# Optimization experiments

Measured on AMD Instinct MI355X. Metric: run time of the kernel, lower is better.

## Reference

```python
import jax, jax.numpy as jnp
import numpy as np
from jax import lax

TIME_DIM = 100   # time_feat_dim
MEM_DIM = 172    # node_feat_dim == memory_dim
TAU = 0.3        # energy_threshold
LAM = 0.01       # softshrink sparsity_threshold


def _layer_norm(x, w, b, eps=1e-5):
    m = x.mean(-1, keepdims=True)
    v = ((x - m) ** 2).mean(-1, keepdims=True)
    return (x - m) / jnp.sqrt(v + eps) * w + b


def _time_encode(t):
    # TGN time encoder: cos(t * 1/10^linspace(0,9,D)), fixed (non-trainable)
    freqs = 1.0 / (10.0 ** jnp.linspace(0.0, 9.0, TIME_DIM))
    return jnp.cos(t[..., None] * freqs)


def _softshrink(x, lam=LAM):
    return jnp.where(x > lam, x - lam, jnp.where(x < -lam, x + lam, 0.0))


def setup_inputs() -> dict:
    key = jax.random.key(0)
    ks = jax.random.split(key, 12)
    B, N, NUM_NODES = 8192, 32, 500000
    s = 0.02  # scale used by Global_Local_Filtering
    return {
        "node_ids": jnp.arange(B, dtype=jnp.int32),
        "neighbor_node_ids": jax.random.randint(ks[0], (B, N), 0, NUM_NODES, dtype=jnp.int32),
        "node_interact_times": jax.random.uniform(ks[1], (B,), dtype=jnp.float32) * 1000.0,
        "neighbor_times": jax.random.uniform(ks[2], (B, N), dtype=jnp.float32) * 1000.0,
        "node_memories": jnp.zeros((NUM_NODES, MEM_DIM), jnp.float32),
        "r1": s * jax.random.normal(ks[3], (TIME_DIM, MEM_DIM), jnp.float32),
        "i1": s * jax.random.normal(ks[4], (TIME_DIM, MEM_DIM), jnp.float32),
        "rb1": s * jax.random.normal(ks[5], (MEM_DIM,), jnp.float32),
        "ib1": s * jax.random.normal(ks[6], (MEM_DIM,), jnp.float32),
        "conv_w": 0.02 * jax.random.normal(ks[7], (MEM_DIM, MEM_DIM, 8), jnp.float32),
        "conv_b": 0.02 * jax.random.normal(ks[8], (MEM_DIM,), jnp.float32),
        "rhythm_w": 0.1 * jax.random.normal(ks[9], (272, 1, 4), jnp.float32),
        "lin_w": 0.05 * jax.random.normal(ks[10], (272, MEM_DIM), jnp.float32),
        "lin_b": 0.02 * jax.random.normal(ks[11], (MEM_DIM,), jnp.float32),
        "mb_ln_w": jnp.ones((MEM_DIM,), jnp.float32),
        "mb_ln_b": jnp.zeros((MEM_DIM,), jnp.float32),
        "ln_w": jnp.ones((MEM_DIM,), jnp.float32),
        "ln_b": jnp.zeros((MEM_DIM,), jnp.float32),
    }


def reference(node_ids, neighbor_node_ids, node_interact_times, neighbor_times,
              node_memories, r1, i1, rb1, ib1, conv_w, conv_b,
              rhythm_w, lin_w, lin_b, mb_ln_w, mb_ln_b, ln_w, ln_b):
    # ---- RhythmMemoryUpdater.update_memory ----
    messages = _time_encode(node_interact_times)                 # [B,100]
    old_mem = node_memories[node_ids]                            # [B,172] gather
    x = jnp.concatenate([messages, old_mem], axis=-1)[:, :, None]  # [B,272,1] (NCH)
    # depthwise Conv1d(272,272,k=4,pad=2,groups=272,no bias): length 1 -> 2
    x = lax.conv_general_dilated(x, rhythm_w, (1,), [(2, 2)],
                                 dimension_numbers=("NCH", "OIH", "NCH"),
                                 feature_group_count=272)        # [B,272,2]
    x = jnp.einsum("bcl,cd->bld", x, lin_w) + lin_b              # [B,2,172]
    new_mem = x.mean(axis=1)                                     # mean(dim=1) since 2 != memory_dim
    # set_memories: layer_norm then scatter; then gather + SeqFilter layernorm
    updated = node_memories.at[node_ids].set(_layer_norm(new_mem, mb_ln_w, mb_ln_b))
    gathered = lax.stop_gradient(updated[node_ids])              # memory bank is non-trainable (no_grad)
    root_node_time = _layer_norm(gathered, ln_w, ln_b)           # [B,172]

    # ---- neighbor branch: FSTS (Global_Local_Filtering + Conv1d) ----
    dt = node_interact_times[:, None] - neighbor_times           # [B,N]
    tfeat = _time_encode(dt)                                     # [B,N,100]
    tfeat = jnp.where((neighbor_node_ids == 0)[..., None], 0.0, tfeat)

    xf = jnp.fft.fft(tfeat, axis=1, norm="ortho")                # [B,N,100] complex
    energy = jnp.sum(jnp.abs(xf) ** 2, axis=-1)                  # [B,N]
    mask = (energy / (energy.mean() + 1e-6) >= TAU).astype(tfeat.dtype)
    low = xf * mask[..., None]
    o_r = jnp.einsum("bnc,cd->bnd", low.real, r1) - jnp.einsum("bnc,cd->bnd", low.imag, i1) + rb1
    o_i = jnp.einsum("bnc,cd->bnd", low.imag, r1) + jnp.einsum("bnc,cd->bnd", low.real, i1) + ib1
    y_fft = _softshrink(jax.nn.relu(o_r)) + 1j * _softshrink(jax.nn.relu(o_i))
    y = jnp.fft.ifft(y_fft, axis=1, norm="ortho").real           # [B,N,172]

    # Local_Correlation: Conv1d(172,172,k=8,pad=4) over neighbor axis, then mean over length
    yc = lax.conv_general_dilated(y.transpose(0, 2, 1), conv_w, (1,), [(4, 4)],
                                  dimension_numbers=("NCH", "OIH", "NCH"))
    yc = yc + conv_b[None, :, None]                              # [B,172,33]
    neighbor_out = yc.mean(axis=-1)                              # [B,172]

    return root_node_time + neighbor_out
```

## Files before the change

### kernel.cpp

```cpp
#include <hip/hip_runtime.h>
#include <hip/hip_bf16.h>
#include <math.h>

#define B_ 8192
#define NN 32
#define TD 100
#define MD 172
#define KD 1376
#define TAUC 0.3f
#define LAMC 0.01f

typedef __attribute__((ext_vector_type(8))) short short8;
typedef __attribute__((ext_vector_type(4))) float f32x4;

#define WS_U_OFF    256
#define U_BYTES     ((size_t)B_ * KD * 2)
#define CONVB_ELEMS (11 * 43 * 64 * 8)
#define WBIG_ELEMS  (22 * 7 * 64 * 8)
#define CS_ELEMS    (2 * 64 * 8)
#define ROOT_ELEMS  (11 * 9 * 64 * 8)
#define CS2_ELEMS   (4 * 64 * 8)
#define FRAG_SHORTS (CONVB_ELEMS + WBIG_ELEMS + CS_ELEMS + ROOT_ELEMS + CS2_ELEMS)
#define TBL_ELEMS   164

__device__ __forceinline__ float wred(float v) {
#pragma unroll
  for (int o = 32; o > 0; o >>= 1) v += __shfl_down(v, o, 64);
  return v;
}

__device__ __forceinline__ short bf16_bits(float f) {
  __hip_bfloat16 h = __float2bfloat16(f);
  return *(short*)&h;
}

__device__ __forceinline__ unsigned pack2(float a, float b) {
  return (unsigned)(unsigned short)bf16_bits(a) |
         ((unsigned)(unsigned short)bf16_bits(b) << 16);
}

__device__ __forceinline__ float fcos(float x) {
  float r = x * 0.15915494309189535f;
  r = r - floorf(r);
  return __builtin_amdgcn_cosf(r);
}

__global__ __launch_bounds__(256) void k_prep0(
    const float* __restrict__ conv_w, const float* __restrict__ r1,
    const float* __restrict__ i1, const float* __restrict__ rhythm_w,
    const float* __restrict__ lin_w, short* __restrict__ convB,
    short* __restrict__ Wfrag, short* __restrict__ CSfrag,
    short* __restrict__ Rfrag, short* __restrict__ CS2frag,
    float* __restrict__ tbl) {
  int idx = blockIdx.x * 256 + threadIdx.x;
  const float inv_s = 0.17677669529663687f;
  if (idx < CONVB_ELEMS) {
    int j = idx & 7;
    int l = (idx >> 3) & 63;
    int s = (idx >> 9) % 43;
    int n0 = idx / (43 * 64 * 8);
    int k = s * 32 + (l >> 4) * 8 + j;
    int col = n0 * 16 + (l & 15);
    float v = (col < MD) ? conv_w[(long)col * KD + k] : 0.f;
    convB[idx] = bf16_bits(v);
    return;
  }
  idx -= CONVB_ELEMS;
  if (idx < WBIG_ELEMS) {
    int j = idx & 7;
    int l = (idx >> 3) & 63;
    int s = (idx % 3584) >> 9;
    int n0 = idx / 3584;
    int k = s * 32 + (l >> 4) * 8 + j;
    int col = n0 * 16 + (l & 15);
    float v = 0.f;
    if (k < 200) {
      if (n0 < 11) {
        int d = col;
        if (d < MD) v = (k < 100) ? r1[k * MD + d] : -i1[(k - 100) * MD + d];
      } else {
        int d = col - 176;
        if (d >= 0 && d < MD) v = (k < 100) ? i1[k * MD + d] : r1[(k - 100) * MD + d];
      }
    }
    Wfrag[idx] = bf16_bits(v);
    return;
  }
  idx -= WBIG_ELEMS;
  if (idx < CS_ELEMS) {
    int j = idx & 7;
    int l = (idx >> 3) & 63;
    int s = idx >> 9;
    int row = l & 15;
    int kq = s * 32 + (l >> 4) * 8 + j;
    float v = 0.f;
    if (row < 8) {
      int kp = (kq < 32) ? kq : kq - 32;
      int lo = row - 4; if (lo < 0) lo = 0;
      int hi = row + 28; if (hi > 31) hi = 31;
      double cs = 0.0, ss = 0.0;
      for (int n = lo; n <= hi; ++n) {
        double ang = 0.19634954084936207740 * (double)((kp * n) & 31);
        cs += cos(ang); ss += sin(ang);
      }
      v = ((kq < 32) ? (float)cs : -(float)ss) * inv_s;
    }
    CSfrag[idx] = bf16_bits(v);
    return;
  }
  idx -= CS_ELEMS;
  if (idx < ROOT_ELEMS) {
    int n = idx / 4608;
    int rem = idx % 4608;
    int s = rem >> 9;
    int l = (rem >> 3) & 63;
    int j = rem & 7;
    int k = s * 32 + (l >> 4) * 8 + j;
    int col = n * 16 + (l & 15);
    float v = 0.f;
    if (k < 272 && col < MD) {
      float hw = 0.5f * (rhythm_w[k * 4 + 1] + rhythm_w[k * 4 + 2]);
      v = hw * lin_w[k * MD + col];
    }
    Rfrag[idx] = bf16_bits(v);
    return;
  }
  idx -= ROOT_ELEMS;
  if (idx < CS2_ELEMS) {
    int set = idx >> 9, l = (idx >> 3) & 63, j = idx & 7;
    int mt = set >> 1, isS = set & 1;
    int kf = mt * 16 + (l & 15);
    int n = ((l >> 4) << 3) + j;
    double ang = 0.19634954084936207740 * (double)((kf * n) & 31);
    double v = isS ? -sin(ang) : cos(ang);
    CS2frag[idx] = bf16_bits((float)(v * 0.1767766952966368811));
    return;
  }
  idx -= CS2_ELEMS;
  if (idx < TBL_ELEMS) {
    float v;
    if (idx < 100)      v = (float)exp(-9.0 * (double)idx / 99.0 * 2.302585092994045684);
    else if (idx < 132) v = (float)cos(0.19634954084936207740 * (double)(idx - 100));
    else                v = (float)sin(0.19634954084936207740 * (double)(idx - 132));
    tbl[idx] = v;
  }
}

__global__ __launch_bounds__(256) void k_mean(const int* __restrict__ nid,
                                              const float* __restrict__ t,
                                              const float* __restrict__ nt,
                                              const float* __restrict__ tbl,
                                              float* __restrict__ ws) {
  __shared__ float fr[TD];
  __shared__ float part[4];
  int tid = threadIdx.x;
  if (tid < TD) fr[tid] = tbl[tid];
  __syncthreads();
  int idx = blockIdx.x * 256 + tid;
  int b = idx >> 5;
  float s = 0.f;
  if (nid[idx] != 0) {
    float dt = t[b] - nt[idx];
    for (int c = 0; c < TD; ++c) { float v = fcos(dt * fr[c]); s = fmaf(v, v, s); }
  }
  s = wred(s);
  if ((tid & 63) == 0) part[tid >> 6] = s;
  __syncthreads();
  if (tid == 0) atomicAdd(ws, part[0] + part[1] + part[2] + part[3]);
}

__global__ __launch_bounds__(384, 8) void k_main(
    const int* __restrict__ nbr_id, const float* __restrict__ t,
    const float* __restrict__ nt, const float* __restrict__ rb1,
    const float* __restrict__ ib1, const float* __restrict__ ws0,
    const short* __restrict__ Wfrag, const short* __restrict__ CSfrag,
    const short* __restrict__ CS2frag, const float* __restrict__ tbl,
    short* __restrict__ u_out) {
  __shared__ __align__(16) short sA[32 * 232];
  __shared__ __align__(16) unsigned char s_un[12800];
  __shared__ float s_fr[TD];
  __shared__ float s_dt[32], s_z[32];
  __shared__ float s_energy[32];

  short* sB = (short*)s_un;
  short* Y = (short*)s_un;
  const int tid = threadIdx.x;
  const int b = blockIdx.x;
  const int l = tid & 63, w = tid >> 6;
  const int c = l & 15, q = l >> 4;

  if (tid < 32) {
    int gi = b * NN + tid;
    int id = nbr_id[gi];
    float d = t[b] - nt[gi];
    s_z[tid]  = (id == 0) ? 0.f : 1.f;
    s_dt[tid] = (id == 0) ? 0.f : d;
    s_energy[tid] = 0.f;
  }
  if (tid < TD) s_fr[tid] = tbl[tid];
  __syncthreads();

  for (int idx = tid; idx < 3584; idx += 384) {
    int tt = idx >> 9, ll = (idx >> 3) & 63, j = idx & 7;
    int n = ((ll >> 4) << 3) + j;
    int cc = (tt << 4) + (ll & 15);
    float v = (cc < TD) ? s_z[n] * fcos(s_dt[n] * s_fr[cc]) : 0.f;
    sB[idx] = bf16_bits(v);
  }
  if (tid < 256) {
    int row = tid >> 3, qq = tid & 7;
    *(uint2*)(sA + row * 232 + 200 + qq * 4) = make_uint2(0u, 0u);
  }
  __syncthreads();

  const int mside = (w >= 3) ? 1 : 0;
  const int wn = w % 3;
  {
    short8 Ac = *(const short8*)(CS2frag + (((mside << 1) + 0) << 9) + (l << 3));
    short8 As = *(const short8*)(CS2frag + (((mside << 1) + 1) << 9) + (l << 3));
    float e4[4] = {0.f, 0.f, 0.f, 0.f};
    for (int tt = wn; tt < 7; tt += 3) {
      short8 Bt = *(const short8*)(sB + (tt << 9) + (l << 3));
      f32x4 xr = (f32x4)(0.f), xi = (f32x4)(0.f);
      xr = __builtin_amdgcn_mfma_f32_16x16x32_bf16(Ac, Bt, xr, 0, 0, 0);
      xi = __builtin_amdgcn_mfma_f32_16x16x32_bf16(As, Bt, xi, 0, 0, 0);
      int cc = (tt << 4) + c;
      if (cc < TD) {
#pragma unroll
        for (int r = 0; r < 4; ++r) {
          int k = mside * 16 + q * 4 + r;
          sA[k * 232 + cc]       = bf16_bits(xr[r]);
          sA[k * 232 + 100 + cc] = bf16_bits(xi[r]);
          e4[r] = fmaf(xr[r], xr[r], e4[r]);
          e4[r] = fmaf(xi[r], xi[r], e4[r]);
        }
      }
    }
#pragma unroll
    for (int m = 1; m < 16; m <<= 1) {
#pragma unroll
      for (int r = 0; r < 4; ++r) e4[r] += __shfl_xor(e4[r], m, 64);
    }
    if (c == 0) {
#pragma unroll
      for (int r = 0; r < 4; ++r)
        atomicAdd(&s_energy[mside * 16 + q * 4 + r], e4[r]);
    }
  }
  __syncthreads();

  {
    float gth = TAUC * (ws0[0] * (1.0f / 262144.0f) + 1e-6f);
    for (int idx = tid; idx < 800; idx += 384) {
      int row = idx / 25, qq = idx - row * 25;
      if (s_energy[row] < gth)
        *(uint4*)((char*)sA + row * 464 + qq * 16) = make_uint4(0u,0u,0u,0u);
    }
  }
  __syncthreads();

#pragma unroll
  for (int rep = 0; rep < 2; ++rep) {
    int n = w + 6 * rep;
    if (n < 11) {
      f32x4 acc0 = (f32x4)(0.f), acc1 = (f32x4)(0.f);
#pragma unroll
      for (int s = 0; s < 7; ++s) {
        short8 bb = *(const short8*)(Wfrag + (((n * 7 + s) << 6) + l) * 8);
        short8 a0 = *(const short8*)(sA + c * 232 + (q << 3) + s * 32);
        short8 a1 = *(const short8*)(sA + (16 + c) * 232 + (q << 3) + s * 32);
        acc0 = __builtin_amdgcn_mfma_f32_16x16x32_bf16(a0, bb, acc0, 0, 0, 0);
        acc1 = __builtin_amdgcn_mfma_f32_16x16x32_bf16(a1, bb, acc1, 0, 0, 0);
      }
      int d = n * 16 + c;
      bool valid = (d < MD);
      float bias = valid ? rb1[d] : 0.f;
      f32x4 y0, y1;
#pragma unroll
      for (int r = 0; r < 4; ++r) {
        y0[r] = valid ? fmaxf(acc0[r] + bias - LAMC, 0.f) : 0.f;
        y1[r] = valid ? fmaxf(acc1[r] + bias - LAMC, 0.f) : 0.f;
      }
      *(uint2*)(Y + d * 32 + (q << 2))      = make_uint2(pack2(y0[0], y0[1]), pack2(y0[2], y0[3]));
      *(uint2*)(Y + d * 32 + 16 + (q << 2)) = make_uint2(pack2(y1[0], y1[1]), pack2(y1[2], y1[3]));
    }
  }
  __syncthreads();

  f32x4 uacc[2];
  uacc[0] = (f32x4)(0.f); uacc[1] = (f32x4)(0.f);
  {
    short8 cs0 = *(const short8*)(CSfrag + (l << 3));
#pragma unroll
    for (int ti = 0; ti < 2; ++ti) {
      int nu = w + 6 * ti;
      if (nu < 11) {
        short8 bfr = *(const short8*)(Y + (nu * 16 + c) * 32 + (q << 3));
        uacc[ti] = __builtin_amdgcn_mfma_f32_16x16x32_bf16(cs0, bfr, uacc[ti], 0, 0, 0);
      }
    }
  }
  __syncthreads();

#pragma unroll
  for (int rep = 0; rep < 2; ++rep) {
    int n = w + 6 * rep;
    if (n < 11) {
      int nw = n + 11;
      f32x4 acc0 = (f32x4)(0.f), acc1 = (f32x4)(0.f);
#pragma unroll
      for (int s = 0; s < 7; ++s) {
        short8 bb = *(const short8*)(Wfrag + (((nw * 7 + s) << 6) + l) * 8);
        short8 a0 = *(const short8*)(sA + c * 232 + (q << 3) + s * 32);
        short8 a1 = *(const short8*)(sA + (16 + c) * 232 + (q << 3) + s * 32);
        acc0 = __builtin_amdgcn_mfma_f32_16x16x32_bf16(a0, bb, acc0, 0, 0, 0);
        acc1 = __builtin_amdgcn_mfma_f32_16x16x32_bf16(a1, bb, acc1, 0, 0, 0);
      }
      int d = n * 16 + c;
      bool valid = (d < MD);
      float bias = valid ? ib1[d] : 0.f;
      f32x4 y0, y1;
#pragma unroll
      for (int r = 0; r < 4; ++r) {
        y0[r] = valid ? fmaxf(acc0[r] + bias - LAMC, 0.f) : 0.f;
        y1[r] = valid ? fmaxf(acc1[r] + bias - LAMC, 0.f) : 0.f;
      }
      *(uint2*)(Y + d * 32 + (q << 2))      = make_uint2(pack2(y0[0], y0[1]), pack2(y0[2], y0[3]));
      *(uint2*)(Y + d * 32 + 16 + (q << 2)) = make_uint2(pack2(y1[0], y1[1]), pack2(y1[2], y1[3]));
    }
  }
  __syncthreads();

  {
    short8 cs1 = *(const short8*)(CSfrag + ((64 + l) << 3));
#pragma unroll
    for (int ti = 0; ti < 2; ++ti) {
      int nu = w + 6 * ti;
      if (nu < 11) {
        short8 bfr = *(const short8*)(Y + (nu * 16 + c) * 32 + (q << 3));
        uacc[ti] = __builtin_amdgcn_mfma_f32_16x16x32_bf16(cs1, bfr, uacc[ti], 0, 0, 0);
        int d = nu * 16 + c;
        if (q < 2 && d < MD) {
          uint2 pv = make_uint2(pack2(uacc[ti][0], uacc[ti][1]),
                                pack2(uacc[ti][2], uacc[ti][3]));
          *(uint2*)(u_out + (long)b * KD + d * 8 + q * 4) = pv;
        }
      }
    }
  }
}

__global__ __launch_bounds__(1024) void k_tail(
    const int* __restrict__ node_ids, const float* __restrict__ t,
    const float* __restrict__ node_mem, const short* __restrict__ u,
    const short* __restrict__ convB, const float* __restrict__ conv_b,
    const short* __restrict__ Rfrag, const float* __restrict__ lin_b,
    const float* __restrict__ mb_w, const float* __restrict__ mb_b,
    const float* __restrict__ ln_w, const float* __restrict__ ln_b,
    const float* __restrict__ tbl, float* __restrict__ out) {
  __shared__ __align__(16) short aR[16 * 296];
  __shared__ __align__(16) float Ct[16 * 176];
  const int tid = threadIdx.x;
  const int l = tid & 63, w = tid >> 6;
  const int c = l & 15, q = l >> 4;
  const int b0 = blockIdx.x * 16;

  for (int idx = tid; idx < 16 * 296; idx += 1024) {
    int r = idx / 296, cc = idx - r * 296;
    float v = 0.f;
    if (cc < TD) v = fcos(t[b0 + r] * tbl[cc]);
    else if (cc < 272) v = node_mem[(long)node_ids[b0 + r] * MD + (cc - TD)];
    aR[idx] = bf16_bits(v);
  }
  __syncthreads();

  f32x4 cacc = (f32x4)(0.f);
  if (w < 11) {
    const short* ap = u + (long)(b0 + c) * KD + (q << 3);
    const short* bp = convB + (((long)w * 43) * 64 + l) * 8;
#pragma unroll 4
    for (int s = 0; s < 43; ++s) {
      short8 a = *(const short8*)(ap + s * 32);
      short8 bb = *(const short8*)(bp + (s << 9));
      cacc = __builtin_amdgcn_mfma_f32_16x16x32_bf16(a, bb, cacc, 0, 0, 0);
    }
  } else {
    const int rstart = (w - 11) * 2;
    const int rcnt = (w == 15) ? 3 : 2;
    f32x4 racc[3];
#pragma unroll
    for (int tt = 0; tt < 3; ++tt) racc[tt] = (f32x4)(0.f);
    const short* arp = aR + c * 296 + (q << 3);
    for (int s = 0; s < 9; ++s) {
      short8 a = *(const short8*)(arp + s * 32);
#pragma unroll
      for (int tt = 0; tt < 3; ++tt) {
        if (tt < rcnt) {
          int n = rstart + tt;
          short8 bb = *(const short8*)(Rfrag + (((n * 9 + s) * 64) + l) * 8);
          racc[tt] = __builtin_amdgcn_mfma_f32_16x16x32_bf16(a, bb, racc[tt], 0, 0, 0);
        }
      }
    }
#pragma unroll
    for (int tt = 0; tt < 3; ++tt) {
      if (tt < rcnt) {
        int n = (rstart + tt) * 16 + c;
#pragma unroll
        for (int r = 0; r < 4; ++r)
          Ct[(q * 4 + r) * 176 + n] = racc[tt][r];
      }
    }
  }
  __syncthreads();

  if (tid < 256) {
    int r = tid >> 4, g = tid & 15;
    float v[11];
    float sm = 0.f, sq = 0.f;
#pragma unroll
    for (int j = 0; j < 11; ++j) {
      int cc = g + 16 * j;
      float x = (cc < MD) ? (Ct[r * 176 + cc] + lin_b[cc]) : 0.f;
      v[j] = x; sm += x; sq += x * x;
    }
#pragma unroll
    for (int m = 1; m < 16; m <<= 1) { sm += __shfl_xor(sm, m, 64); sq += __shfl_xor(sq, m, 64); }
    float mean = sm / 172.f;
    float rstd = rsqrtf(sq / 172.f - mean * mean + 1e-5f);
    float sm2 = 0.f, sq2 = 0.f;
#pragma unroll
    for (int j = 0; j < 11; ++j) {
      int cc = g + 16 * j;
      if (cc < MD) {
        float h = (v[j] - mean) * rstd * mb_w[cc] + mb_b[cc];
        v[j] = h; sm2 += h; sq2 += h * h;
      }
    }
#pragma unroll
    for (int m = 1; m < 16; m <<= 1) { sm2 += __shfl_xor(sm2, m, 64); sq2 += __shfl_xor(sq2, m, 64); }
    float mean2 = sm2 / 172.f;
    float rstd2 = rsqrtf(sq2 / 172.f - mean2 * mean2 + 1e-5f);
#pragma unroll
    for (int j = 0; j < 11; ++j) {
      int cc = g + 16 * j;
      if (cc < MD) Ct[r * 176 + cc] = (v[j] - mean2) * rstd2 * ln_w[cc] + ln_b[cc];
    }
  }
  __syncthreads();

  if (w < 11) {
    int n = w * 16 + c;
    if (n < MD) {
      float cb = conv_b[n];
#pragma unroll
      for (int r = 0; r < 4; ++r) {
        int mr = q * 4 + r;
        out[(long)(b0 + mr) * MD + n] =
            Ct[mr * 176 + n] + cacc[r] * (1.0f / 33.0f) + cb;
      }
    }
  }
}

extern "C" void kernel_launch(void* const* d_in, const int* in_sizes, int n_in,
                              void* d_out, int out_size, void* d_ws, size_t ws_size,
                              hipStream_t stream) {
  const int* node_ids = (const int*)d_in[0];
  const int* nbr_id   = (const int*)d_in[1];
  const float* t  = (const float*)d_in[2];
  const float* nt = (const float*)d_in[3];
  const float* node_mem = (const float*)d_in[4];
  const float* r1 = (const float*)d_in[5];
  const float* i1 = (const float*)d_in[6];
  const float* rb1 = (const float*)d_in[7];
  const float* ib1 = (const float*)d_in[8];
  const float* conv_w = (const float*)d_in[9];
  const float* conv_b = (const float*)d_in[10];
  const float* rhythm_w = (const float*)d_in[11];
  const float* lin_w = (const float*)d_in[12];
  const float* lin_b = (const float*)d_in[13];
  const float* mb_w = (const float*)d_in[14];
  const float* mb_b = (const float*)d_in[15];
  const float* ln_w = (const float*)d_in[16];
  const float* ln_b = (const float*)d_in[17];
  float* out = (float*)d_out;
  float* wsf = (float*)d_ws;

  char* base = (char*)d_ws;
  short* u       = (short*)(base + WS_U_OFF);
  short* convB   = (short*)(base + WS_U_OFF + U_BYTES);
  short* Wfrag   = convB + CONVB_ELEMS;
  short* CSfrag  = Wfrag + WBIG_ELEMS;
  short* Rfrag   = CSfrag + CS_ELEMS;
  short* CS2frag = Rfrag + ROOT_ELEMS;
  float* tbl     = (float*)(CS2frag + CS2_ELEMS);

  hipMemsetAsync(d_ws, 0, 16, stream);
  k_prep0<<<(FRAG_SHORTS + TBL_ELEMS + 255) / 256, 256, 0, stream>>>(
      conv_w, r1, i1, rhythm_w, lin_w, convB, Wfrag, CSfrag, Rfrag, CS2frag, tbl);
  k_mean<<<1024, 256, 0, stream>>>(nbr_id, t, nt, tbl, wsf);
  k_main<<<B_, 384, 0, stream>>>(nbr_id, t, nt, rb1, ib1, wsf,
                                 Wfrag, CSfrag, CS2frag, tbl, u);
  k_tail<<<512, 1024, 0, stream>>>(node_ids, t, node_mem, u, convB, conv_b,
                                   Rfrag, lin_b, mb_w, mb_b, ln_w, ln_b, tbl, out);
}
```

Baseline: 565.1 us.

## Fuse real/imag spectral GEMMs with fp32 cos/sin reduction and merge prep kernels

The prep and energy-mean kernels are merged into one launch, with the mean blocks computing their frequency table inline. In the main kernel, the real and imaginary output GEMMs now run in a single pass with four accumulators. The inverse-DFT-plus-conv-window projection is done in registers: an fp32 dot product against a shared-memory cos/sin table, then cross-lane shuffles. This removes the bf16 Y staging buffer, two block barriers and two small MFMA stages, in exchange for more registers per thread and extra shuffles.

```diff
diff --git a/kernel.cpp b/kernel.cpp
--- a/kernel.cpp
+++ b/kernel.cpp
@@ -17,11 +17,12 @@
 #define U_BYTES     ((size_t)B_ * KD * 2)
 #define CONVB_ELEMS (11 * 43 * 64 * 8)
 #define WBIG_ELEMS  (22 * 7 * 64 * 8)
-#define CS_ELEMS    (2 * 64 * 8)
 #define ROOT_ELEMS  (11 * 9 * 64 * 8)
 #define CS2_ELEMS   (4 * 64 * 8)
-#define FRAG_SHORTS (CONVB_ELEMS + WBIG_ELEMS + CS_ELEMS + ROOT_ELEMS + CS2_ELEMS)
-#define TBL_ELEMS   164
+#define TBL_ELEMS   676
+#define PREP_ITEMS  (CONVB_ELEMS + WBIG_ELEMS + ROOT_ELEMS + CS2_ELEMS + TBL_ELEMS)
+#define MEAN_BLOCKS 1024
+#define PREP_BLOCKS ((PREP_ITEMS + 255) / 256)
 
 __device__ __forceinline__ float wred(float v) {
 #pragma unroll
@@ -45,15 +46,36 @@
   return __builtin_amdgcn_cosf(r);
 }
 
-__global__ __launch_bounds__(256) void k_prep0(
+__global__ __launch_bounds__(256) void k_pm(
+    const int* __restrict__ nid, const float* __restrict__ t,
+    const float* __restrict__ nt,
     const float* __restrict__ conv_w, const float* __restrict__ r1,
     const float* __restrict__ i1, const float* __restrict__ rhythm_w,
     const float* __restrict__ lin_w, short* __restrict__ convB,
-    short* __restrict__ Wfrag, short* __restrict__ CSfrag,
-    short* __restrict__ Rfrag, short* __restrict__ CS2frag,
-    float* __restrict__ tbl) {
-  int idx = blockIdx.x * 256 + threadIdx.x;
+    short* __restrict__ Wfrag, short* __restrict__ Rfrag,
+    short* __restrict__ CS2frag, float* __restrict__ tbl,
+    float* __restrict__ ws) {
   const float inv_s = 0.17677669529663687f;
+  const int tid = threadIdx.x;
+  if (blockIdx.x < MEAN_BLOCKS) {
+    __shared__ float fr[TD];
+    __shared__ float part[4];
+    if (tid < TD) fr[tid] = (float)exp(-9.0 * (double)tid / 99.0 * 2.302585092994045684);
+    __syncthreads();
+    int idx = blockIdx.x * 256 + tid;
+    int b = idx >> 5;
+    float s = 0.f;
+    if (nid[idx] != 0) {
+      float dt = t[b] - nt[idx];
+      for (int c = 0; c < TD; ++c) { float v = fcos(dt * fr[c]); s = fmaf(v, v, s); }
+    }
+    s = wred(s);
+    if ((tid & 63) == 0) part[tid >> 6] = s;
+    __syncthreads();
+    if (tid == 0) atomicAdd(ws, part[0] + part[1] + part[2] + part[3]);
+    return;
+  }
+  int idx = (blockIdx.x - MEAN_BLOCKS) * 256 + tid;
   if (idx < CONVB_ELEMS) {
     int j = idx & 7;
     int l = (idx >> 3) & 63;
@@ -87,28 +109,6 @@
     return;
   }
   idx -= WBIG_ELEMS;
-  if (idx < CS_ELEMS) {
-    int j = idx & 7;
-    int l = (idx >> 3) & 63;
-    int s = idx >> 9;
-    int row = l & 15;
-    int kq = s * 32 + (l >> 4) * 8 + j;
-    float v = 0.f;
-    if (row < 8) {
-      int kp = (kq < 32) ? kq : kq - 32;
-      int lo = row - 4; if (lo < 0) lo = 0;
-      int hi = row + 28; if (hi > 31) hi = 31;
-      double cs = 0.0, ss = 0.0;
-      for (int n = lo; n <= hi; ++n) {
-        double ang = 0.19634954084936207740 * (double)((kp * n) & 31);
-        cs += cos(ang); ss += sin(ang);
-      }
-      v = ((kq < 32) ? (float)cs : -(float)ss) * inv_s;
-    }
-    CSfrag[idx] = bf16_bits(v);
-    return;
-  }
-  idx -= CS_ELEMS;
   if (idx < ROOT_ELEMS) {
     int n = idx / 4608;
     int rem = idx % 4608;
@@ -141,49 +141,37 @@
     float v;
     if (idx < 100)      v = (float)exp(-9.0 * (double)idx / 99.0 * 2.302585092994045684);
     else if (idx < 132) v = (float)cos(0.19634954084936207740 * (double)(idx - 100));
-    else                v = (float)sin(0.19634954084936207740 * (double)(idx - 132));
+    else if (idx < 164) v = (float)sin(0.19634954084936207740 * (double)(idx - 132));
+    else {
+      int i2 = idx - 164;
+      int half = (i2 >= 256) ? 1 : 0;
+      int r = i2 & 255;
+      int k2 = r >> 5, kp = r & 31;
+      int lo = k2 - 4; if (lo < 0) lo = 0;
+      int hi = k2 + 28; if (hi > 31) hi = 31;
+      double cs = 0.0, ss = 0.0;
+      for (int n = lo; n <= hi; ++n) {
+        double ang = 0.19634954084936207740 * (double)((kp * n) & 31);
+        cs += cos(ang); ss += sin(ang);
+      }
+      v = (half ? (float)ss : (float)cs) * inv_s;
+    }
     tbl[idx] = v;
   }
-}
-
-__global__ __launch_bounds__(256) void k_mean(const int* __restrict__ nid,
-                                              const float* __restrict__ t,
-                                              const float* __restrict__ nt,
-                                              const float* __restrict__ tbl,
-                                              float* __restrict__ ws) {
-  __shared__ float fr[TD];
-  __shared__ float part[4];
-  int tid = threadIdx.x;
-  if (tid < TD) fr[tid] = tbl[tid];
-  __syncthreads();
-  int idx = blockIdx.x * 256 + tid;
-  int b = idx >> 5;
-  float s = 0.f;
-  if (nid[idx] != 0) {
-    float dt = t[b] - nt[idx];
-    for (int c = 0; c < TD; ++c) { float v = fcos(dt * fr[c]); s = fmaf(v, v, s); }
-  }
-  s = wred(s);
-  if ((tid & 63) == 0) part[tid >> 6] = s;
-  __syncthreads();
-  if (tid == 0) atomicAdd(ws, part[0] + part[1] + part[2] + part[3]);
 }
 
 __global__ __launch_bounds__(384, 8) void k_main(
     const int* __restrict__ nbr_id, const float* __restrict__ t,
     const float* __restrict__ nt, const float* __restrict__ rb1,
     const float* __restrict__ ib1, const float* __restrict__ ws0,
-    const short* __restrict__ Wfrag, const short* __restrict__ CSfrag,
-    const short* __restrict__ CS2frag, const float* __restrict__ tbl,
-    short* __restrict__ u_out) {
+    const short* __restrict__ Wfrag, const short* __restrict__ CS2frag,
+    const float* __restrict__ tbl, short* __restrict__ u_out) {
   __shared__ __align__(16) short sA[32 * 232];
-  __shared__ __align__(16) unsigned char s_un[12800];
+  __shared__ __align__(16) short sB[3584];
+  __shared__ __align__(16) float s_cs[512];
   __shared__ float s_fr[TD];
-  __shared__ float s_dt[32], s_z[32];
-  __shared__ float s_energy[32];
-
-  short* sB = (short*)s_un;
-  short* Y = (short*)s_un;
+  __shared__ float s_dt[32], s_z[32], s_energy[32];
+
   const int tid = threadIdx.x;
   const int b = blockIdx.x;
   const int l = tid & 63, w = tid >> 6;
@@ -198,6 +186,7 @@
     s_energy[tid] = 0.f;
   }
   if (tid < TD) s_fr[tid] = tbl[tid];
+  for (int i = tid; i < 512; i += 384) s_cs[i] = tbl[164 + i];
   __syncthreads();
 
   for (int idx = tid; idx < 3584; idx += 384) {
@@ -263,88 +252,56 @@
   for (int rep = 0; rep < 2; ++rep) {
     int n = w + 6 * rep;
     if (n < 11) {
-      f32x4 acc0 = (f32x4)(0.f), acc1 = (f32x4)(0.f);
+      f32x4 aR0 = (f32x4)(0.f), aR1 = (f32x4)(0.f);
+      f32x4 aI0 = (f32x4)(0.f), aI1 = (f32x4)(0.f);
 #pragma unroll
       for (int s = 0; s < 7; ++s) {
-        short8 bb = *(const short8*)(Wfrag + (((n * 7 + s) << 6) + l) * 8);
+        short8 br = *(const short8*)(Wfrag + (((n * 7 + s) << 6) + l) * 8);
+        short8 bi = *(const short8*)(Wfrag + ((((n + 11) * 7 + s) << 6) + l) * 8);
         short8 a0 = *(const short8*)(sA + c * 232 + (q << 3) + s * 32);
         short8 a1 = *(const short8*)(sA + (16 + c) * 232 + (q << 3) + s * 32);
-        acc0 = __builtin_amdgcn_mfma_f32_16x16x32_bf16(a0, bb, acc0, 0, 0, 0);
-        acc1 = __builtin_amdgcn_mfma_f32_16x16x32_bf16(a1, bb, acc1, 0, 0, 0);
+        aR0 = __builtin_amdgcn_mfma_f32_16x16x32_bf16(a0, br, aR0, 0, 0, 0);
+        aR1 = __builtin_amdgcn_mfma_f32_16x16x32_bf16(a1, br, aR1, 0, 0, 0);
+        aI0 = __builtin_amdgcn_mfma_f32_16x16x32_bf16(a0, bi, aI0, 0, 0, 0);
+        aI1 = __builtin_amdgcn_mfma_f32_16x16x32_bf16(a1, bi, aI1, 0, 0, 0);
       }
       int d = n * 16 + c;
       bool valid = (d < MD);
-      float bias = valid ? rb1[d] : 0.f;
-      f32x4 y0, y1;
+      float br_ = valid ? rb1[d] : 0.f;
+      float bi_ = valid ? ib1[d] : 0.f;
 #pragma unroll
       for (int r = 0; r < 4; ++r) {
-        y0[r] = valid ? fmaxf(acc0[r] + bias - LAMC, 0.f) : 0.f;
-        y1[r] = valid ? fmaxf(acc1[r] + bias - LAMC, 0.f) : 0.f;
-      }
-      *(uint2*)(Y + d * 32 + (q << 2))      = make_uint2(pack2(y0[0], y0[1]), pack2(y0[2], y0[3]));
-      *(uint2*)(Y + d * 32 + 16 + (q << 2)) = make_uint2(pack2(y1[0], y1[1]), pack2(y1[2], y1[3]));
-    }
-  }
-  __syncthreads();
-
-  f32x4 uacc[2];
-  uacc[0] = (f32x4)(0.f); uacc[1] = (f32x4)(0.f);
-  {
-    short8 cs0 = *(const short8*)(CSfrag + (l << 3));
-#pragma unroll
-    for (int ti = 0; ti < 2; ++ti) {
-      int nu = w + 6 * ti;
-      if (nu < 11) {
-        short8 bfr = *(const short8*)(Y + (nu * 16 + c) * 32 + (q << 3));
-        uacc[ti] = __builtin_amdgcn_mfma_f32_16x16x32_bf16(cs0, bfr, uacc[ti], 0, 0, 0);
-      }
-    }
-  }
-  __syncthreads();
-
-#pragma unroll
-  for (int rep = 0; rep < 2; ++rep) {
-    int n = w + 6 * rep;
-    if (n < 11) {
-      int nw = n + 11;
-      f32x4 acc0 = (f32x4)(0.f), acc1 = (f32x4)(0.f);
-#pragma unroll
-      for (int s = 0; s < 7; ++s) {
-        short8 bb = *(const short8*)(Wfrag + (((nw * 7 + s) << 6) + l) * 8);
-        short8 a0 = *(const short8*)(sA + c * 232 + (q << 3) + s * 32);
-        short8 a1 = *(const short8*)(sA + (16 + c) * 232 + (q << 3) + s * 32);
-        acc0 = __builtin_amdgcn_mfma_f32_16x16x32_bf16(a0, bb, acc0, 0, 0, 0);
-        acc1 = __builtin_amdgcn_mfma_f32_16x16x32_bf16(a1, bb, acc1, 0, 0, 0);
-      }
-      int d = n * 16 + c;
-      bool valid = (d < MD);
-      float bias = valid ? ib1[d] : 0.f;
-      f32x4 y0, y1;
-#pragma unroll
-      for (int r = 0; r < 4; ++r) {
-        y0[r] = valid ? fmaxf(acc0[r] + bias - LAMC, 0.f) : 0.f;
-        y1[r] = valid ? fmaxf(acc1[r] + bias - LAMC, 0.f) : 0.f;
-      }
-      *(uint2*)(Y + d * 32 + (q << 2))      = make_uint2(pack2(y0[0], y0[1]), pack2(y0[2], y0[3]));
-      *(uint2*)(Y + d * 32 + 16 + (q << 2)) = make_uint2(pack2(y1[0], y1[1]), pack2(y1[2], y1[3]));
-    }
-  }
-  __syncthreads();
-
-  {
-    short8 cs1 = *(const short8*)(CSfrag + ((64 + l) << 3));
-#pragma unroll
-    for (int ti = 0; ti < 2; ++ti) {
-      int nu = w + 6 * ti;
-      if (nu < 11) {
-        short8 bfr = *(const short8*)(Y + (nu * 16 + c) * 32 + (q << 3));
-        uacc[ti] = __builtin_amdgcn_mfma_f32_16x16x32_bf16(cs1, bfr, uacc[ti], 0, 0, 0);
-        int d = nu * 16 + c;
-        if (q < 2 && d < MD) {
-          uint2 pv = make_uint2(pack2(uacc[ti][0], uacc[ti][1]),
-                                pack2(uacc[ti][2], uacc[ti][3]));
-          *(uint2*)(u_out + (long)b * KD + d * 8 + q * 4) = pv;
+        aR0[r] = fmaxf(aR0[r] + br_ - LAMC, 0.f);
+        aR1[r] = fmaxf(aR1[r] + br_ - LAMC, 0.f);
+        aI0[r] = fmaxf(aI0[r] + bi_ - LAMC, 0.f);
+        aI1[r] = fmaxf(aI1[r] + bi_ - LAMC, 0.f);
+      }
+      float uk[8];
+#pragma unroll
+      for (int k2 = 0; k2 < 8; ++k2) {
+        f32x4 ct0 = *(const f32x4*)(s_cs + k2 * 32 + (q << 2));
+        f32x4 ct1 = *(const f32x4*)(s_cs + k2 * 32 + 16 + (q << 2));
+        f32x4 st0 = *(const f32x4*)(s_cs + 256 + k2 * 32 + (q << 2));
+        f32x4 st1 = *(const f32x4*)(s_cs + 256 + k2 * 32 + 16 + (q << 2));
+        float sacc = 0.f;
+#pragma unroll
+        for (int r = 0; r < 4; ++r) {
+          sacc = fmaf(ct0[r],  aR0[r], sacc);
+          sacc = fmaf(ct1[r],  aR1[r], sacc);
+          sacc = fmaf(st0[r], -aI0[r], sacc);
+          sacc = fmaf(st1[r], -aI1[r], sacc);
         }
+        uk[k2] = sacc;
+      }
+#pragma unroll
+      for (int k2 = 0; k2 < 8; ++k2) {
+        uk[k2] += __shfl_xor(uk[k2], 16, 64);
+        uk[k2] += __shfl_xor(uk[k2], 32, 64);
+      }
+      if (q == 0 && valid) {
+        uint4 pv = make_uint4(pack2(uk[0], uk[1]), pack2(uk[2], uk[3]),
+                              pack2(uk[4], uk[5]), pack2(uk[6], uk[7]));
+        *(uint4*)(u_out + (long)b * KD + d * 8) = pv;
       }
     }
   }
@@ -491,17 +448,16 @@
   short* u       = (short*)(base + WS_U_OFF);
   short* convB   = (short*)(base + WS_U_OFF + U_BYTES);
   short* Wfrag   = convB + CONVB_ELEMS;
-  short* CSfrag  = Wfrag + WBIG_ELEMS;
-  short* Rfrag   = CSfrag + CS_ELEMS;
+  short* Rfrag   = Wfrag + WBIG_ELEMS;
   short* CS2frag = Rfrag + ROOT_ELEMS;
   float* tbl     = (float*)(CS2frag + CS2_ELEMS);
 
   hipMemsetAsync(d_ws, 0, 16, stream);
-  k_prep0<<<(FRAG_SHORTS + TBL_ELEMS + 255) / 256, 256, 0, stream>>>(
-      conv_w, r1, i1, rhythm_w, lin_w, convB, Wfrag, CSfrag, Rfrag, CS2frag, tbl);
-  k_mean<<<1024, 256, 0, stream>>>(nbr_id, t, nt, tbl, wsf);
+  k_pm<<<MEAN_BLOCKS + PREP_BLOCKS, 256, 0, stream>>>(
+      nbr_id, t, nt, conv_w, r1, i1, rhythm_w, lin_w,
+      convB, Wfrag, Rfrag, CS2frag, tbl, wsf);
   k_main<<<B_, 384, 0, stream>>>(nbr_id, t, nt, rb1, ib1, wsf,
-                                 Wfrag, CSfrag, CS2frag, tbl, u);
+                                 Wfrag, CS2frag, tbl, u);
   k_tail<<<512, 1024, 0, stream>>>(node_ids, t, node_mem, u, convB, conv_b,
                                    Rfrag, lin_b, mb_w, mb_b, ln_w, ln_b, tbl, out);
 }
```

Measured after the change: 1.509 ms. +167.0%, slower.
